# Optimization experiments

Hardware: AMD Instinct MI355X
Metric: run time of the kernel (lower is better)

## Reference

```python
import jax, jax.numpy as jnp
import numpy as np

BN_EPS = 1e-5
HEADS = 8

def _bn(y, gamma, beta, mean, var):
    # eval-mode BatchNorm2d over channel axis 1; y: [B,C,H,W]
    scale = gamma / jnp.sqrt(var + BN_EPS)
    shift = beta - mean * scale
    return y * scale[None, :, None, None] + shift[None, :, None, None]

def setup_inputs() -> dict:
    key = jax.random.key(0)
    ks = jax.random.split(key, 12)
    B, C, H, W = 16, 256, 64, 64
    x = jax.random.normal(ks[0], (B, C, H, W), jnp.float32)
    qkv_w = jax.random.normal(ks[1], (3 * C, C), jnp.float32) * 0.05
    qkv_gamma = jax.random.uniform(ks[2], (3 * C,), jnp.float32, 0.5, 1.5)
    qkv_beta = jax.random.normal(ks[3], (3 * C,), jnp.float32) * 0.1
    qkv_mean = jax.random.normal(ks[4], (3 * C,), jnp.float32) * 0.1
    qkv_var = jax.random.uniform(ks[5], (3 * C,), jnp.float32, 0.5, 1.5)
    proj_w = jax.random.normal(ks[6], (C, C), jnp.float32) * 0.05
    proj_gamma = jax.random.uniform(ks[7], (C,), jnp.float32, 0.5, 1.5)
    proj_beta = jax.random.normal(ks[8], (C,), jnp.float32) * 0.1
    proj_mean = jax.random.normal(ks[9], (C,), jnp.float32) * 0.1
    proj_var = jax.random.uniform(ks[10], (C,), jnp.float32, 0.5, 1.5)
    return {"x": x, "qkv_w": qkv_w, "qkv_gamma": qkv_gamma, "qkv_beta": qkv_beta,
            "qkv_mean": qkv_mean, "qkv_var": qkv_var, "proj_w": proj_w,
            "proj_gamma": proj_gamma, "proj_beta": proj_beta,
            "proj_mean": proj_mean, "proj_var": proj_var}

def reference(x, qkv_w, qkv_gamma, qkv_beta, qkv_mean, qkv_var,
              proj_w, proj_gamma, proj_beta, proj_mean, proj_var):
    B, C, H, W = x.shape
    hd = C // HEADS  # head_dim
    # 1x1 conv (no bias) + BN
    qkv = jnp.einsum('bchw,oc->bohw', x, qkv_w)
    qkv = _bn(qkv, qkv_gamma, qkv_beta, qkv_mean, qkv_var)
    q, k, v = jnp.split(qkv, 3, axis=1)
    N = H * W
    q = q.reshape(B, HEADS, hd, N)
    k = k.reshape(B, HEADS, hd, N)
    v = v.reshape(B, HEADS, hd, N)
    q = jax.nn.softmax(q, axis=-1)   # over tokens
    k = jax.nn.softmax(k, axis=-2)   # over head_dim
    context = jnp.einsum('bhdn,bhen->bhde', k, v)   # [B,h,d,d]
    out = jnp.einsum('bhdn,bhde->bhen', q, context) # [B,h,d,N]
    out = out.reshape(B, C, H, W)
    out = jnp.einsum('bchw,oc->bohw', out, proj_w)
    out = _bn(out, proj_gamma, proj_beta, proj_mean, proj_var)
    return out
```

## Files before the change

kernel.cpp:

```cpp
#include <hip/hip_runtime.h>

typedef unsigned short ushort_t;
typedef unsigned int u32;
typedef short short8 __attribute__((ext_vector_type(8)));
typedef float f32x4 __attribute__((ext_vector_type(4)));
typedef float f32x16 __attribute__((ext_vector_type(16)));

#define NTOK 4096
#define NCOLS 65536
#define CIN 256

__device__ __forceinline__ float b2f(ushort_t u) {
    union { unsigned int i; float f; } v; v.i = ((unsigned int)u) << 16; return v.f;
}
__device__ __forceinline__ ushort_t f2b(float f) {
    union { float f; unsigned int i; } v; v.f = f;
    unsigned int r = v.i + 0x7FFFu + ((v.i >> 16) & 1u);
    return (ushort_t)(r >> 16);
}

__device__ __forceinline__ void gl_lds16(const ushort_t* g, ushort_t* l) {
    __builtin_amdgcn_global_load_lds(
        (const __attribute__((address_space(1))) u32*)(const void*)g,
        (__attribute__((address_space(3))) u32*)(void*)l,
        16, 0, 0);
}

__global__ __launch_bounds__(256) void cvt_w(const float* __restrict__ wq,
                                             const float* __restrict__ wp,
                                             ushort_t* __restrict__ wqb,
                                             ushort_t* __restrict__ wpb,
                                             float* __restrict__ ctxz) {
    int i = blockIdx.x * 256 + threadIdx.x;
    if (i < 768 * 256) wqb[i] = f2b(wq[i]);
    else               wpb[i - 768 * 256] = f2b(wp[i - 768 * 256]);
    if (i < 131072) ctxz[i] = 0.f;
}

__global__ __launch_bounds__(256) void transpose_x(const float* __restrict__ x,
                                                   ushort_t* __restrict__ xt) {
    int tl = threadIdx.x & 63, cg = threadIdx.x >> 6;
    int g = blockIdx.x * 64 + tl;
    int b = g >> 12, n = g & 4095;
    const float* src = x + (size_t)b * (CIN * NTOK) + n;
    ushort_t* dst = xt + (size_t)g * CIN + cg * 64;
    for (int j8 = 0; j8 < 8; j8++) {
        short8 vr;
#pragma unroll
        for (int j = 0; j < 8; j++)
            vr[j] = (short)f2b(src[(size_t)(cg * 64 + j8 * 8 + j) * NTOK]);
        *(short8*)(dst + j8 * 8) = vr;
    }
}

__global__ __launch_bounds__(256) void gemm128(const ushort_t* __restrict__ W,
                                               const ushort_t* __restrict__ Xc,
                                               const float* __restrict__ gamma,
                                               const float* __restrict__ beta,
                                               const float* __restrict__ mean,
                                               const float* __restrict__ var,
                                               ushort_t* __restrict__ out_b,
                                               float* __restrict__ out_f, int mode) {
    __shared__ __align__(16) ushort_t lA[128 * 32];
    __shared__ __align__(16) ushort_t lB[128 * 32];
    int tid = threadIdx.x;
    int wave = tid >> 6, lane = tid & 63;
    int l15 = lane & 15, q = lane >> 4;
    int mh = wave >> 1, nh = wave & 1;
    int m0 = blockIdx.y * 128, colb = blockIdx.x * 128;

    f32x4 acc[4][4];
#pragma unroll
    for (int i = 0; i < 4; i++)
#pragma unroll
        for (int j = 0; j < 4; j++)
#pragma unroll
            for (int r = 0; r < 4; r++) acc[i][j][r] = 0.f;

    const ushort_t* gA0 = W  + (size_t)(m0 +      (tid >> 2)) * CIN + (tid & 3) * 8;
    const ushort_t* gA1 = W  + (size_t)(m0 + 64 + (tid >> 2)) * CIN + (tid & 3) * 8;
    const ushort_t* gB0 = Xc + (size_t)(colb +      (tid >> 2)) * CIN + (tid & 3) * 8;
    const ushort_t* gB1 = Xc + (size_t)(colb + 64 + (tid >> 2)) * CIN + (tid & 3) * 8;
    ushort_t* la0 = &lA[tid * 8];
    ushort_t* la1 = &lA[2048 + tid * 8];
    ushort_t* lb0 = &lB[tid * 8];
    ushort_t* lb1 = &lB[2048 + tid * 8];

    for (int k0 = 0; k0 < CIN; k0 += 32) {
        gl_lds16(gA0 + k0, la0);
        gl_lds16(gA1 + k0, la1);
        gl_lds16(gB0 + k0, lb0);
        gl_lds16(gB1 + k0, lb1);
        __syncthreads();
        short8 af[4], bf[4];
#pragma unroll
        for (int i = 0; i < 4; i++) {
            af[i] = *(const short8*)&lA[(mh * 64 + i * 16 + l15) * 32 + q * 8];
            bf[i] = *(const short8*)&lB[(nh * 64 + i * 16 + l15) * 32 + q * 8];
        }
#pragma unroll
        for (int mi = 0; mi < 4; mi++)
#pragma unroll
            for (int ni = 0; ni < 4; ni++)
                acc[mi][ni] = __builtin_amdgcn_mfma_f32_16x16x32_bf16(af[mi], bf[ni],
                                                                      acc[mi][ni], 0, 0, 0);
        __syncthreads();
    }

    int col_l = colb + nh * 64 + l15;
#pragma unroll
    for (int mi = 0; mi < 4; mi++) {
#pragma unroll
        for (int r = 0; r < 4; r++) {
            int m = m0 + mh * 64 + mi * 16 + q * 4 + r;
            float sc = gamma[m] * rsqrtf(var[m] + 1e-5f);
            float sh = beta[m] - mean[m] * sc;
#pragma unroll
            for (int ni = 0; ni < 4; ni++) {
                float val = acc[mi][ni][r] * sc + sh;
                int col = col_l + ni * 16;
                if (mode == 0) {
                    out_b[(size_t)m * NCOLS + col] = f2b(val);
                } else {
                    int bb = col >> 12, n = col & 4095;
                    out_f[(size_t)bb * (CIN * NTOK) + (size_t)m * NTOK + n] = val;
                }
            }
        }
    }
}

__global__ __launch_bounds__(256) void softmax_qk(ushort_t* __restrict__ qkv) {
    int bx = blockIdx.x;
    int tid = threadIdx.x, wave = tid >> 6, lane = tid & 63;
    if (bx < 1024) {
        int rid = bx * 4 + wave;
        int c = rid >> 4, b = rid & 15;
        ushort_t* row = qkv + (size_t)c * NCOLS + b * NTOK;
        float v[64];
#pragma unroll
        for (int j = 0; j < 8; j++) {
            short8 pk = *(const short8*)(row + j * 512 + lane * 8);
#pragma unroll
            for (int i = 0; i < 8; i++) v[j * 8 + i] = b2f((ushort_t)pk[i]);
        }
        float m = v[0];
#pragma unroll
        for (int i = 1; i < 64; i++) m = fmaxf(m, v[i]);
        for (int off = 1; off < 64; off <<= 1) m = fmaxf(m, __shfl_xor(m, off));
        float s = 0.f;
#pragma unroll
        for (int i = 0; i < 64; i++) { v[i] = __expf(v[i] - m); s += v[i]; }
        for (int off = 1; off < 64; off <<= 1) s += __shfl_xor(s, off);
        float inv = 1.f / s;
#pragma unroll
        for (int j = 0; j < 8; j++) {
            short8 pk;
#pragma unroll
            for (int i = 0; i < 8; i++) pk[i] = (short)f2b(v[j * 8 + i] * inv);
            *(short8*)(row + j * 512 + lane * 8) = pk;
        }
    } else {
        int idx = bx - 1024;
        int h = idx >> 7, chunk = idx & 127;
        int col = chunk * 512 + tid * 2;
        ushort_t* base = qkv + (size_t)(256 + h * 32) * NCOLS + col;
        float v0[32], v1[32];
#pragma unroll
        for (int d = 0; d < 32; d++) {
            u32 pk = *(const u32*)(base + (size_t)d * NCOLS);
            v0[d] = b2f((ushort_t)(pk & 0xFFFF));
            v1[d] = b2f((ushort_t)(pk >> 16));
        }
        float m0 = v0[0], m1 = v1[0];
#pragma unroll
        for (int d = 1; d < 32; d++) { m0 = fmaxf(m0, v0[d]); m1 = fmaxf(m1, v1[d]); }
        float s0 = 0.f, s1 = 0.f;
#pragma unroll
        for (int d = 0; d < 32; d++) {
            v0[d] = __expf(v0[d] - m0); s0 += v0[d];
            v1[d] = __expf(v1[d] - m1); s1 += v1[d];
        }
        float i0 = 1.f / s0, i1 = 1.f / s1;
#pragma unroll
        for (int d = 0; d < 32; d++) {
            u32 pk = (u32)f2b(v0[d] * i0) | ((u32)f2b(v1[d] * i1) << 16);
            *(u32*)(base + (size_t)d * NCOLS) = pk;
        }
    }
}

__global__ __launch_bounds__(256) void ctx_ker(const ushort_t* __restrict__ qkv,
                                               float* __restrict__ ctxbuf) {
    int s = blockIdx.x, bh = blockIdx.y;
    int b = bh >> 3, h = bh & 7;
    int tid = threadIdx.x, wave = tid >> 6, lane = tid & 63;
    int l31 = lane & 31, l5 = lane >> 5;
    int col0 = b * NTOK + s * 512 + wave * 128;
    const ushort_t* krow = qkv + (size_t)(256 + h * 32 + l31) * NCOLS + col0 + l5 * 8;
    const ushort_t* vrow = qkv + (size_t)(512 + h * 32 + l31) * NCOLS + col0 + l5 * 8;
    f32x16 acc;
#pragma unroll
    for (int i = 0; i < 16; i++) acc[i] = 0.f;
#pragma unroll
    for (int st = 0; st < 8; st++) {
        short8 af = *(const short8*)(krow + st * 16);
        short8 bf = *(const short8*)(vrow + st * 16);
        acc = __builtin_amdgcn_mfma_f32_32x32x16_bf16(af, bf, acc, 0, 0, 0);
    }
    __shared__ float red[4][1024];
#pragma unroll
    for (int r = 0; r < 16; r++) {
        int d = (r & 3) + 8 * (r >> 2) + 4 * l5;
        red[wave][d * 32 + l31] = acc[r];
    }
    __syncthreads();
    int i0 = tid * 4;
#pragma unroll
    for (int i = 0; i < 4; i++) {
        int idx = i0 + i;
        float v = red[0][idx] + red[1][idx] + red[2][idx] + red[3][idx];
        atomicAdd(ctxbuf + (size_t)bh * 1024 + idx, v);
    }
}

__global__ __launch_bounds__(256) void out_ker(const ushort_t* __restrict__ qkv,
                                               const float* __restrict__ ctxbuf,
                                               ushort_t* __restrict__ attT) {
    int s = blockIdx.x, bh = blockIdx.y;
    int b = bh >> 3, h = bh & 7;
    int tid = threadIdx.x, wave = tid >> 6, lane = tid & 63;
    int l31 = lane & 31, l5 = lane >> 5;
    __shared__ __align__(16) ushort_t ctxT[32 * 40];
    __shared__ __align__(16) ushort_t qT[256 * 40];
    __shared__ __align__(16) ushort_t obuf[4][32 * 40];

#pragma unroll
    for (int i = 0; i < 4; i++) {
        int idx = tid * 4 + i;
        int d = idx >> 5, e = idx & 31;
        ctxT[e * 40 + d] = f2b(ctxbuf[(size_t)bh * 1024 + idx]);
    }
    __syncthreads();
    short8 a0 = *(const short8*)(ctxT + l31 * 40 + l5 * 8);
    short8 a1 = *(const short8*)(ctxT + l31 * 40 + 16 + l5 * 8);

    const ushort_t* qbase = qkv + (size_t)(h * 32) * NCOLS;
    int segbase = b * NTOK + s * 512;

    for (int nc = 0; nc < 2; nc++) {
        int gcol0 = segbase + nc * 256;
        int d = tid & 31, t8 = (tid >> 5) * 8;
#pragma unroll
        for (int jj = 0; jj < 4; jj++) {
            int tok8 = jj * 64 + t8;
            short8 pk = *(const short8*)(qbase + (size_t)d * NCOLS + gcol0 + tok8);
#pragma unroll
            for (int j = 0; j < 8; j++) qT[(tok8 + j) * 40 + d] = (ushort_t)pk[j];
        }
        __syncthreads();
#pragma unroll
        for (int ti = 0; ti < 2; ti++) {
            int tok0 = (wave + ti * 4) * 32;
            f32x16 acc;
#pragma unroll
            for (int i = 0; i < 16; i++) acc[i] = 0.f;
            short8 b0 = *(const short8*)(qT + (size_t)(tok0 + l31) * 40 + l5 * 8);
            short8 b1 = *(const short8*)(qT + (size_t)(tok0 + l31) * 40 + 16 + l5 * 8);
            acc = __builtin_amdgcn_mfma_f32_32x32x16_bf16(a0, b0, acc, 0, 0, 0);
            acc = __builtin_amdgcn_mfma_f32_32x32x16_bf16(a1, b1, acc, 0, 0, 0);
#pragma unroll
            for (int r = 0; r < 16; r++) {
                int e = (r & 3) + 8 * (r >> 2) + 4 * l5;
                obuf[wave][l31 * 40 + e] = f2b(acc[r]);
            }
            __syncthreads();
            {
                int tok = lane >> 1, half = lane & 1;
                const ushort_t* srcp = &obuf[wave][tok * 40 + half * 16];
                short8 r0 = *(const short8*)srcp;
                short8 r1 = *(const short8*)(srcp + 8);
                size_t g = (size_t)(gcol0 + tok0 + tok) * 256 + h * 32 + half * 16;
                *(short8*)(attT + g) = r0;
                *(short8*)(attT + g + 8) = r1;
            }
            __syncthreads();
        }
        __syncthreads();
    }
}

extern "C" void kernel_launch(void* const* d_in, const int* in_sizes, int n_in,
                              void* d_out, int out_size, void* d_ws, size_t ws_size,
                              hipStream_t stream) {
    const float* x          = (const float*)d_in[0];
    const float* qkv_w      = (const float*)d_in[1];
    const float* qkv_gamma  = (const float*)d_in[2];
    const float* qkv_beta   = (const float*)d_in[3];
    const float* qkv_mean   = (const float*)d_in[4];
    const float* qkv_var    = (const float*)d_in[5];
    const float* proj_w     = (const float*)d_in[6];
    const float* proj_gamma = (const float*)d_in[7];
    const float* proj_beta  = (const float*)d_in[8];
    const float* proj_mean  = (const float*)d_in[9];
    const float* proj_var   = (const float*)d_in[10];

    ushort_t* wqb = (ushort_t*)d_ws;
    ushort_t* wpb = wqb + 768 * 256;
    ushort_t* xt  = wpb + 256 * 256;
    ushort_t* qkv = xt + (size_t)NCOLS * CIN;
    float* out    = (float*)d_out;
    float* ctxbuf = (float*)d_out;

    cvt_w<<<1024, 256, 0, stream>>>(qkv_w, proj_w, wqb, wpb, ctxbuf);
    transpose_x<<<1024, 256, 0, stream>>>(x, xt);
    gemm128<<<dim3(512, 6), 256, 0, stream>>>(wqb, xt, qkv_gamma, qkv_beta,
                                              qkv_mean, qkv_var, qkv, nullptr, 0);
    softmax_qk<<<2048, 256, 0, stream>>>(qkv);
    ctx_ker<<<dim3(8, 128), 256, 0, stream>>>(qkv, ctxbuf);
    out_ker<<<dim3(8, 128), 256, 0, stream>>>(qkv, ctxbuf, xt);
    gemm128<<<dim3(512, 2), 256, 0, stream>>>(wpb, xt, proj_gamma, proj_beta,
                                              proj_mean, proj_var, nullptr, out, 1);
}
```

Measured before the change: 305.1 us.

## Fuse q/k softmax into QKV GEMM epilogue and defer q normalization

Removes the separate softmax_qk kernel. The k softmax over head_dim is computed in the QKV GEMM epilogue with cross-lane shuffles. For q, exp is taken without max subtraction and per-row sums are accumulated with atomics, and the division is folded into the context matrix in out_ker. The GEMM operand roles are swapped so the epilogue can write vectorized 4-element stores along tokens. This saves a full read/write pass over q and k, but dropping the max subtraction risks overflow for large logits.

```diff
diff --git a/kernel.cpp b/kernel.cpp
--- a/kernel.cpp
+++ b/kernel.cpp
@@ -3,6 +3,7 @@
 typedef unsigned short ushort_t;
 typedef unsigned int u32;
 typedef short short8 __attribute__((ext_vector_type(8)));
+typedef short short4_t __attribute__((ext_vector_type(4)));
 typedef float f32x4 __attribute__((ext_vector_type(4)));
 typedef float f32x16 __attribute__((ext_vector_type(16)));
 
@@ -30,11 +31,11 @@
                                              const float* __restrict__ wp,
                                              ushort_t* __restrict__ wqb,
                                              ushort_t* __restrict__ wpb,
-                                             float* __restrict__ ctxz) {
+                                             float* __restrict__ scz) {
     int i = blockIdx.x * 256 + threadIdx.x;
     if (i < 768 * 256) wqb[i] = f2b(wq[i]);
     else               wpb[i - 768 * 256] = f2b(wp[i - 768 * 256]);
-    if (i < 131072) ctxz[i] = 0.f;
+    if (i < 131072 + 4096) scz[i] = 0.f;
 }
 
 __global__ __launch_bounds__(256) void transpose_x(const float* __restrict__ x,
@@ -60,13 +61,14 @@
                                                const float* __restrict__ mean,
                                                const float* __restrict__ var,
                                                ushort_t* __restrict__ out_b,
-                                               float* __restrict__ out_f, int mode) {
+                                               float* __restrict__ out_f,
+                                               float* __restrict__ qsums, int mode) {
     __shared__ __align__(16) ushort_t lA[128 * 32];
     __shared__ __align__(16) ushort_t lB[128 * 32];
     int tid = threadIdx.x;
     int wave = tid >> 6, lane = tid & 63;
     int l15 = lane & 15, q = lane >> 4;
-    int mh = wave >> 1, nh = wave & 1;
+    int th = wave >> 1, ch = wave & 1;
     int m0 = blockIdx.y * 128, colb = blockIdx.x * 128;
 
     f32x4 acc[4][4];
@@ -95,108 +97,117 @@
         short8 af[4], bf[4];
 #pragma unroll
         for (int i = 0; i < 4; i++) {
-            af[i] = *(const short8*)&lA[(mh * 64 + i * 16 + l15) * 32 + q * 8];
-            bf[i] = *(const short8*)&lB[(nh * 64 + i * 16 + l15) * 32 + q * 8];
-        }
-#pragma unroll
-        for (int mi = 0; mi < 4; mi++)
-#pragma unroll
-            for (int ni = 0; ni < 4; ni++)
-                acc[mi][ni] = __builtin_amdgcn_mfma_f32_16x16x32_bf16(af[mi], bf[ni],
-                                                                      acc[mi][ni], 0, 0, 0);
+            af[i] = *(const short8*)&lB[(th * 64 + i * 16 + l15) * 32 + q * 8];
+            bf[i] = *(const short8*)&lA[(ch * 64 + i * 16 + l15) * 32 + q * 8];
+        }
+#pragma unroll
+        for (int ti = 0; ti < 4; ti++)
+#pragma unroll
+            for (int ci = 0; ci < 4; ci++)
+                acc[ti][ci] = __builtin_amdgcn_mfma_f32_16x16x32_bf16(af[ti], bf[ci],
+                                                                      acc[ti][ci], 0, 0, 0);
         __syncthreads();
     }
 
-    int col_l = colb + nh * 64 + l15;
-#pragma unroll
-    for (int mi = 0; mi < 4; mi++) {
-#pragma unroll
-        for (int r = 0; r < 4; r++) {
-            int m = m0 + mh * 64 + mi * 16 + q * 4 + r;
-            float sc = gamma[m] * rsqrtf(var[m] + 1e-5f);
-            float sh = beta[m] - mean[m] * sc;
-#pragma unroll
-            for (int ni = 0; ni < 4; ni++) {
-                float val = acc[mi][ni][r] * sc + sh;
-                int col = col_l + ni * 16;
-                if (mode == 0) {
-                    out_b[(size_t)m * NCOLS + col] = f2b(val);
-                } else {
-                    int bb = col >> 12, n = col & 4095;
-                    out_f[(size_t)bb * (CIN * NTOK) + (size_t)m * NTOK + n] = val;
+    float s[4], sh[4];
+    int mch[4];
+#pragma unroll
+    for (int ci = 0; ci < 4; ci++) {
+        int m = m0 + ch * 64 + ci * 16 + l15;
+        mch[ci] = m;
+        s[ci] = gamma[m] * rsqrtf(var[m] + 1e-5f);
+        sh[ci] = beta[m] - mean[m] * s[ci];
+    }
+    int tb = colb + th * 64;
+    int y = blockIdx.y;
+
+    if (mode == 1) {
+        int bb = colb >> 12;
+#pragma unroll
+        for (int ti = 0; ti < 4; ti++) {
+            int n0 = ((tb + ti * 16 + q * 4) & 4095);
+#pragma unroll
+            for (int ci = 0; ci < 4; ci++) {
+                f32x4 v;
+#pragma unroll
+                for (int r = 0; r < 4; r++) v[r] = acc[ti][ci][r] * s[ci] + sh[ci];
+                *(f32x4*)(out_f + (size_t)bb * (CIN * NTOK) + (size_t)mch[ci] * NTOK + n0) = v;
+            }
+        }
+    } else if (y >= 4) {
+#pragma unroll
+        for (int ti = 0; ti < 4; ti++) {
+            int t0 = tb + ti * 16 + q * 4;
+#pragma unroll
+            for (int ci = 0; ci < 4; ci++) {
+                short4_t pk;
+#pragma unroll
+                for (int r = 0; r < 4; r++) pk[r] = (short)f2b(acc[ti][ci][r] * s[ci] + sh[ci]);
+                *(short4_t*)(out_b + (size_t)mch[ci] * NCOLS + t0) = pk;
+            }
+        }
+    } else if (y >= 2) {
+#pragma unroll
+        for (int ti = 0; ti < 4; ti++) {
+            int t0 = tb + ti * 16 + q * 4;
+#pragma unroll
+            for (int hp = 0; hp < 2; hp++) {
+                int c0 = 2 * hp, c1 = 2 * hp + 1;
+                float e0[4], e1[4];
+                short4_t p0, p1;
+#pragma unroll
+                for (int r = 0; r < 4; r++) {
+                    e0[r] = __expf(acc[ti][c0][r] * s[c0] + sh[c0]);
+                    e1[r] = __expf(acc[ti][c1][r] * s[c1] + sh[c1]);
+                    float t = e0[r] + e1[r];
+                    t += __shfl_xor(t, 1);
+                    t += __shfl_xor(t, 2);
+                    t += __shfl_xor(t, 4);
+                    t += __shfl_xor(t, 8);
+                    float inv = 1.f / t;
+                    p0[r] = (short)f2b(e0[r] * inv);
+                    p1[r] = (short)f2b(e1[r] * inv);
                 }
-            }
-        }
-    }
-}
-
-__global__ __launch_bounds__(256) void softmax_qk(ushort_t* __restrict__ qkv) {
-    int bx = blockIdx.x;
-    int tid = threadIdx.x, wave = tid >> 6, lane = tid & 63;
-    if (bx < 1024) {
-        int rid = bx * 4 + wave;
-        int c = rid >> 4, b = rid & 15;
-        ushort_t* row = qkv + (size_t)c * NCOLS + b * NTOK;
-        float v[64];
-#pragma unroll
-        for (int j = 0; j < 8; j++) {
-            short8 pk = *(const short8*)(row + j * 512 + lane * 8);
-#pragma unroll
-            for (int i = 0; i < 8; i++) v[j * 8 + i] = b2f((ushort_t)pk[i]);
-        }
-        float m = v[0];
-#pragma unroll
-        for (int i = 1; i < 64; i++) m = fmaxf(m, v[i]);
-        for (int off = 1; off < 64; off <<= 1) m = fmaxf(m, __shfl_xor(m, off));
-        float s = 0.f;
-#pragma unroll
-        for (int i = 0; i < 64; i++) { v[i] = __expf(v[i] - m); s += v[i]; }
-        for (int off = 1; off < 64; off <<= 1) s += __shfl_xor(s, off);
-        float inv = 1.f / s;
-#pragma unroll
-        for (int j = 0; j < 8; j++) {
-            short8 pk;
-#pragma unroll
-            for (int i = 0; i < 8; i++) pk[i] = (short)f2b(v[j * 8 + i] * inv);
-            *(short8*)(row + j * 512 + lane * 8) = pk;
+                *(short4_t*)(out_b + (size_t)mch[c0] * NCOLS + t0) = p0;
+                *(short4_t*)(out_b + (size_t)mch[c1] * NCOLS + t0) = p1;
+            }
         }
     } else {
-        int idx = bx - 1024;
-        int h = idx >> 7, chunk = idx & 127;
-        int col = chunk * 512 + tid * 2;
-        ushort_t* base = qkv + (size_t)(256 + h * 32) * NCOLS + col;
-        float v0[32], v1[32];
-#pragma unroll
-        for (int d = 0; d < 32; d++) {
-            u32 pk = *(const u32*)(base + (size_t)d * NCOLS);
-            v0[d] = b2f((ushort_t)(pk & 0xFFFF));
-            v1[d] = b2f((ushort_t)(pk >> 16));
-        }
-        float m0 = v0[0], m1 = v1[0];
-#pragma unroll
-        for (int d = 1; d < 32; d++) { m0 = fmaxf(m0, v0[d]); m1 = fmaxf(m1, v1[d]); }
-        float s0 = 0.f, s1 = 0.f;
-#pragma unroll
-        for (int d = 0; d < 32; d++) {
-            v0[d] = __expf(v0[d] - m0); s0 += v0[d];
-            v1[d] = __expf(v1[d] - m1); s1 += v1[d];
-        }
-        float i0 = 1.f / s0, i1 = 1.f / s1;
-#pragma unroll
-        for (int d = 0; d < 32; d++) {
-            u32 pk = (u32)f2b(v0[d] * i0) | ((u32)f2b(v1[d] * i1) << 16);
-            *(u32*)(base + (size_t)d * NCOLS) = pk;
+        int bb = colb >> 12;
+        float part[4] = {0.f, 0.f, 0.f, 0.f};
+#pragma unroll
+        for (int ti = 0; ti < 4; ti++) {
+            int t0 = tb + ti * 16 + q * 4;
+#pragma unroll
+            for (int ci = 0; ci < 4; ci++) {
+                short4_t pk;
+#pragma unroll
+                for (int r = 0; r < 4; r++) {
+                    float e = __expf(acc[ti][ci][r] * s[ci] + sh[ci]);
+                    ushort_t hv = f2b(e);
+                    pk[r] = (short)hv;
+                    part[ci] += b2f(hv);
+                }
+                *(short4_t*)(out_b + (size_t)mch[ci] * NCOLS + t0) = pk;
+            }
+        }
+#pragma unroll
+        for (int ci = 0; ci < 4; ci++) {
+            float p = part[ci];
+            p += __shfl_xor(p, 16);
+            p += __shfl_xor(p, 32);
+            if (q == 0) atomicAdd(qsums + mch[ci] * 16 + bb, p);
         }
     }
 }
 
 __global__ __launch_bounds__(256) void ctx_ker(const ushort_t* __restrict__ qkv,
                                                float* __restrict__ ctxbuf) {
-    int s = blockIdx.x, bh = blockIdx.y;
+    int sl = blockIdx.x, bh = blockIdx.y;
     int b = bh >> 3, h = bh & 7;
     int tid = threadIdx.x, wave = tid >> 6, lane = tid & 63;
     int l31 = lane & 31, l5 = lane >> 5;
-    int col0 = b * NTOK + s * 512 + wave * 128;
+    int col0 = b * NTOK + sl * 512 + wave * 128;
     const ushort_t* krow = qkv + (size_t)(256 + h * 32 + l31) * NCOLS + col0 + l5 * 8;
     const ushort_t* vrow = qkv + (size_t)(512 + h * 32 + l31) * NCOLS + col0 + l5 * 8;
     f32x16 acc;
@@ -226,8 +237,9 @@
 
 __global__ __launch_bounds__(256) void out_ker(const ushort_t* __restrict__ qkv,
                                                const float* __restrict__ ctxbuf,
+                                               const float* __restrict__ qsums,
                                                ushort_t* __restrict__ attT) {
-    int s = blockIdx.x, bh = blockIdx.y;
+    int sl = blockIdx.x, bh = blockIdx.y;
     int b = bh >> 3, h = bh & 7;
     int tid = threadIdx.x, wave = tid >> 6, lane = tid & 63;
     int l31 = lane & 31, l5 = lane >> 5;
@@ -239,14 +251,15 @@
     for (int i = 0; i < 4; i++) {
         int idx = tid * 4 + i;
         int d = idx >> 5, e = idx & 31;
-        ctxT[e * 40 + d] = f2b(ctxbuf[(size_t)bh * 1024 + idx]);
+        float sc = qsums[(h * 32 + d) * 16 + b];
+        ctxT[e * 40 + d] = f2b(ctxbuf[(size_t)bh * 1024 + idx] / sc);
     }
     __syncthreads();
     short8 a0 = *(const short8*)(ctxT + l31 * 40 + l5 * 8);
     short8 a1 = *(const short8*)(ctxT + l31 * 40 + 16 + l5 * 8);
 
     const ushort_t* qbase = qkv + (size_t)(h * 32) * NCOLS;
-    int segbase = b * NTOK + s * 512;
+    int segbase = b * NTOK + sl * 512;
 
     for (int nc = 0; nc < 2; nc++) {
         int gcol0 = segbase + nc * 256;
@@ -311,14 +324,16 @@
     ushort_t* qkv = xt + (size_t)NCOLS * CIN;
     float* out    = (float*)d_out;
     float* ctxbuf = (float*)d_out;
+    float* qsums  = ctxbuf + 131072;
 
     cvt_w<<<1024, 256, 0, stream>>>(qkv_w, proj_w, wqb, wpb, ctxbuf);
     transpose_x<<<1024, 256, 0, stream>>>(x, xt);
     gemm128<<<dim3(512, 6), 256, 0, stream>>>(wqb, xt, qkv_gamma, qkv_beta,
-                                              qkv_mean, qkv_var, qkv, nullptr, 0);
-    softmax_qk<<<2048, 256, 0, stream>>>(qkv);
+                                              qkv_mean, qkv_var, qkv, nullptr,
+                                              qsums, 0);
     ctx_ker<<<dim3(8, 128), 256, 0, stream>>>(qkv, ctxbuf);
-    out_ker<<<dim3(8, 128), 256, 0, stream>>>(qkv, ctxbuf, xt);
+    out_ker<<<dim3(8, 128), 256, 0, stream>>>(qkv, ctxbuf, qsums, xt);
     gemm128<<<dim3(512, 2), 256, 0, stream>>>(wpb, xt, proj_gamma, proj_beta,
-                                              proj_mean, proj_var, nullptr, out, 1);
-}
+                                              proj_mean, proj_var, nullptr, out,
+                                              qsums, 1);
+}
```

Result: slower. 352.5 us (+15.5%).

## Fuse softmaxes into context and output kernels; stage x transpose through LDS

Applied to the files above, without the earlier changes.

Drops the standalone softmax pass that read and rewrote the q and k rows in place. The k softmax over head_dim is now computed inside ctx_ker with cross-lane shuffles before the MFMA. For q, a lighter kernel computes only per-row exp sums, and out_ker applies exp and the reciprocal sum while staging q into LDS. The x transpose now gathers through a padded LDS tile so global reads and writes coalesce. The q softmax skips the max subtraction, so it relies on the BN outputs being small enough that exp does not overflow, and k exps are recomputed per use.

```diff
diff --git a/kernel.cpp b/kernel.cpp
--- a/kernel.cpp
+++ b/kernel.cpp
@@ -3,6 +3,7 @@
 typedef unsigned short ushort_t;
 typedef unsigned int u32;
 typedef short short8 __attribute__((ext_vector_type(8)));
+typedef short short4_t __attribute__((ext_vector_type(4)));
 typedef float f32x4 __attribute__((ext_vector_type(4)));
 typedef float f32x16 __attribute__((ext_vector_type(16)));
 
@@ -30,27 +31,31 @@
                                              const float* __restrict__ wp,
                                              ushort_t* __restrict__ wqb,
                                              ushort_t* __restrict__ wpb,
-                                             float* __restrict__ ctxz) {
+                                             float* __restrict__ scz) {
     int i = blockIdx.x * 256 + threadIdx.x;
     if (i < 768 * 256) wqb[i] = f2b(wq[i]);
     else               wpb[i - 768 * 256] = f2b(wp[i - 768 * 256]);
-    if (i < 131072) ctxz[i] = 0.f;
+    if (i < 131072) scz[i] = 0.f;
 }
 
 __global__ __launch_bounds__(256) void transpose_x(const float* __restrict__ x,
                                                    ushort_t* __restrict__ xt) {
-    int tl = threadIdx.x & 63, cg = threadIdx.x >> 6;
-    int g = blockIdx.x * 64 + tl;
-    int b = g >> 12, n = g & 4095;
-    const float* src = x + (size_t)b * (CIN * NTOK) + n;
-    ushort_t* dst = xt + (size_t)g * CIN + cg * 64;
-    for (int j8 = 0; j8 < 8; j8++) {
-        short8 vr;
-#pragma unroll
-        for (int j = 0; j < 8; j++)
-            vr[j] = (short)f2b(src[(size_t)(cg * 64 + j8 * 8 + j) * NTOK]);
-        *(short8*)(dst + j8 * 8) = vr;
-    }
+    __shared__ ushort_t lds[64 * 264];
+    int tid = threadIdx.x;
+    int g0 = blockIdx.x * 64;
+    int b = g0 >> 12, n0 = g0 & 4095;
+    const float* src = x + (size_t)b * (CIN * NTOK);
+    int tn = tid & 63, cg = tid >> 6;
+    for (int c4 = 0; c4 < 64; c4++) {
+        int c = c4 * 4 + cg;
+        lds[tn * 264 + c] = f2b(src[(size_t)c * NTOK + n0 + tn]);
+    }
+    __syncthreads();
+    int tok = tid >> 2, c8 = (tid & 3) * 8;
+    ushort_t* dst = xt + (size_t)(g0 + tok) * CIN + c8;
+#pragma unroll
+    for (int j = 0; j < 8; j++)
+        *(short8*)(dst + j * 32) = *(const short8*)&lds[tok * 264 + c8 + j * 32];
 }
 
 __global__ __launch_bounds__(256) void gemm128(const ushort_t* __restrict__ W,
@@ -130,73 +135,30 @@
     }
 }
 
-__global__ __launch_bounds__(256) void softmax_qk(ushort_t* __restrict__ qkv) {
-    int bx = blockIdx.x;
+__global__ __launch_bounds__(256) void qsum_ker(const ushort_t* __restrict__ qkv,
+                                                float* __restrict__ qsums) {
     int tid = threadIdx.x, wave = tid >> 6, lane = tid & 63;
-    if (bx < 1024) {
-        int rid = bx * 4 + wave;
-        int c = rid >> 4, b = rid & 15;
-        ushort_t* row = qkv + (size_t)c * NCOLS + b * NTOK;
-        float v[64];
-#pragma unroll
-        for (int j = 0; j < 8; j++) {
-            short8 pk = *(const short8*)(row + j * 512 + lane * 8);
-#pragma unroll
-            for (int i = 0; i < 8; i++) v[j * 8 + i] = b2f((ushort_t)pk[i]);
-        }
-        float m = v[0];
-#pragma unroll
-        for (int i = 1; i < 64; i++) m = fmaxf(m, v[i]);
-        for (int off = 1; off < 64; off <<= 1) m = fmaxf(m, __shfl_xor(m, off));
-        float s = 0.f;
-#pragma unroll
-        for (int i = 0; i < 64; i++) { v[i] = __expf(v[i] - m); s += v[i]; }
-        for (int off = 1; off < 64; off <<= 1) s += __shfl_xor(s, off);
-        float inv = 1.f / s;
-#pragma unroll
-        for (int j = 0; j < 8; j++) {
-            short8 pk;
-#pragma unroll
-            for (int i = 0; i < 8; i++) pk[i] = (short)f2b(v[j * 8 + i] * inv);
-            *(short8*)(row + j * 512 + lane * 8) = pk;
-        }
-    } else {
-        int idx = bx - 1024;
-        int h = idx >> 7, chunk = idx & 127;
-        int col = chunk * 512 + tid * 2;
-        ushort_t* base = qkv + (size_t)(256 + h * 32) * NCOLS + col;
-        float v0[32], v1[32];
-#pragma unroll
-        for (int d = 0; d < 32; d++) {
-            u32 pk = *(const u32*)(base + (size_t)d * NCOLS);
-            v0[d] = b2f((ushort_t)(pk & 0xFFFF));
-            v1[d] = b2f((ushort_t)(pk >> 16));
-        }
-        float m0 = v0[0], m1 = v1[0];
-#pragma unroll
-        for (int d = 1; d < 32; d++) { m0 = fmaxf(m0, v0[d]); m1 = fmaxf(m1, v1[d]); }
-        float s0 = 0.f, s1 = 0.f;
-#pragma unroll
-        for (int d = 0; d < 32; d++) {
-            v0[d] = __expf(v0[d] - m0); s0 += v0[d];
-            v1[d] = __expf(v1[d] - m1); s1 += v1[d];
-        }
-        float i0 = 1.f / s0, i1 = 1.f / s1;
-#pragma unroll
-        for (int d = 0; d < 32; d++) {
-            u32 pk = (u32)f2b(v0[d] * i0) | ((u32)f2b(v1[d] * i1) << 16);
-            *(u32*)(base + (size_t)d * NCOLS) = pk;
-        }
-    }
+    int rid = blockIdx.x * 4 + wave;
+    int c = rid >> 4, b = rid & 15;
+    const ushort_t* row = qkv + (size_t)c * NCOLS + b * NTOK;
+    float s = 0.f;
+#pragma unroll
+    for (int j = 0; j < 8; j++) {
+        short8 pk = *(const short8*)(row + j * 512 + lane * 8);
+#pragma unroll
+        for (int i = 0; i < 8; i++) s += __expf(b2f((ushort_t)pk[i]));
+    }
+    for (int off = 1; off < 64; off <<= 1) s += __shfl_xor(s, off);
+    if (lane == 0) qsums[c * 16 + b] = s;
 }
 
 __global__ __launch_bounds__(256) void ctx_ker(const ushort_t* __restrict__ qkv,
                                                float* __restrict__ ctxbuf) {
-    int s = blockIdx.x, bh = blockIdx.y;
+    int sl = blockIdx.x, bh = blockIdx.y;
     int b = bh >> 3, h = bh & 7;
     int tid = threadIdx.x, wave = tid >> 6, lane = tid & 63;
     int l31 = lane & 31, l5 = lane >> 5;
-    int col0 = b * NTOK + s * 512 + wave * 128;
+    int col0 = b * NTOK + sl * 512 + wave * 128;
     const ushort_t* krow = qkv + (size_t)(256 + h * 32 + l31) * NCOLS + col0 + l5 * 8;
     const ushort_t* vrow = qkv + (size_t)(512 + h * 32 + l31) * NCOLS + col0 + l5 * 8;
     f32x16 acc;
@@ -204,9 +166,21 @@
     for (int i = 0; i < 16; i++) acc[i] = 0.f;
 #pragma unroll
     for (int st = 0; st < 8; st++) {
-        short8 af = *(const short8*)(krow + st * 16);
-        short8 bf = *(const short8*)(vrow + st * 16);
-        acc = __builtin_amdgcn_mfma_f32_32x32x16_bf16(af, bf, acc, 0, 0, 0);
+        short8 kf = *(const short8*)(krow + st * 16);
+        short8 vf = *(const short8*)(vrow + st * 16);
+        short8 af;
+#pragma unroll
+        for (int j = 0; j < 8; j++) {
+            float e = __expf(b2f((ushort_t)kf[j]));
+            float t = e;
+            t += __shfl_xor(t, 1);
+            t += __shfl_xor(t, 2);
+            t += __shfl_xor(t, 4);
+            t += __shfl_xor(t, 8);
+            t += __shfl_xor(t, 16);
+            af[j] = (short)f2b(__fdividef(e, t));
+        }
+        acc = __builtin_amdgcn_mfma_f32_32x32x16_bf16(af, vf, acc, 0, 0, 0);
     }
     __shared__ float red[4][1024];
 #pragma unroll
@@ -226,8 +200,9 @@
 
 __global__ __launch_bounds__(256) void out_ker(const ushort_t* __restrict__ qkv,
                                                const float* __restrict__ ctxbuf,
+                                               const float* __restrict__ qsums,
                                                ushort_t* __restrict__ attT) {
-    int s = blockIdx.x, bh = blockIdx.y;
+    int sl = blockIdx.x, bh = blockIdx.y;
     int b = bh >> 3, h = bh & 7;
     int tid = threadIdx.x, wave = tid >> 6, lane = tid & 63;
     int l31 = lane & 31, l5 = lane >> 5;
@@ -246,17 +221,19 @@
     short8 a1 = *(const short8*)(ctxT + l31 * 40 + 16 + l5 * 8);
 
     const ushort_t* qbase = qkv + (size_t)(h * 32) * NCOLS;
-    int segbase = b * NTOK + s * 512;
+    int segbase = b * NTOK + sl * 512;
+    int d = tid & 31, t8 = (tid >> 5) * 8;
+    float sq = 1.f / qsums[(h * 32 + d) * 16 + b];
 
     for (int nc = 0; nc < 2; nc++) {
         int gcol0 = segbase + nc * 256;
-        int d = tid & 31, t8 = (tid >> 5) * 8;
 #pragma unroll
         for (int jj = 0; jj < 4; jj++) {
             int tok8 = jj * 64 + t8;
             short8 pk = *(const short8*)(qbase + (size_t)d * NCOLS + gcol0 + tok8);
 #pragma unroll
-            for (int j = 0; j < 8; j++) qT[(tok8 + j) * 40 + d] = (ushort_t)pk[j];
+            for (int j = 0; j < 8; j++)
+                qT[(tok8 + j) * 40 + d] = f2b(__expf(b2f((ushort_t)pk[j])) * sq);
         }
         __syncthreads();
 #pragma unroll
@@ -311,14 +288,15 @@
     ushort_t* qkv = xt + (size_t)NCOLS * CIN;
     float* out    = (float*)d_out;
     float* ctxbuf = (float*)d_out;
+    float* qsums  = ctxbuf + 131072;
 
     cvt_w<<<1024, 256, 0, stream>>>(qkv_w, proj_w, wqb, wpb, ctxbuf);
     transpose_x<<<1024, 256, 0, stream>>>(x, xt);
     gemm128<<<dim3(512, 6), 256, 0, stream>>>(wqb, xt, qkv_gamma, qkv_beta,
                                               qkv_mean, qkv_var, qkv, nullptr, 0);
-    softmax_qk<<<2048, 256, 0, stream>>>(qkv);
+    qsum_ker<<<1024, 256, 0, stream>>>(qkv, qsums);
     ctx_ker<<<dim3(8, 128), 256, 0, stream>>>(qkv, ctxbuf);
-    out_ker<<<dim3(8, 128), 256, 0, stream>>>(qkv, ctxbuf, xt);
+    out_ker<<<dim3(8, 128), 256, 0, stream>>>(qkv, ctxbuf, qsums, xt);
     gemm128<<<dim3(512, 2), 256, 0, stream>>>(wpb, xt, proj_gamma, proj_beta,
                                               proj_mean, proj_var, nullptr, out, 1);
 }
```

New measurement: 296.4 us. -2.9%, faster.
